# Kernel tuning notes

Measured on AMD Instinct MI355X. Metric: run time of the kernel, lower is better.

Reference implementation:

```python
import jax, jax.numpy as jnp
import numpy as np

NUM_EXPERTS = 8
EMBED_DIM = 1024
BATCH, SEQ = 4, 2048


def setup_inputs() -> dict:
    key = jax.random.key(0)
    k1, k2, k3 = jax.random.split(key, 3)
    E_symb = jax.random.normal(k1, (BATCH, SEQ, EMBED_DIM), dtype=jnp.float32)
    gate_w = jax.random.normal(k2, (EMBED_DIM, NUM_EXPERTS), dtype=jnp.float32) * 0.02
    gate_b = jnp.zeros((NUM_EXPERTS,), dtype=jnp.float32)
    expert_w = jax.random.normal(k3, (NUM_EXPERTS, EMBED_DIM, EMBED_DIM), dtype=jnp.float32) * 0.02
    return {"E_symb": E_symb, "gate_w": gate_w, "gate_b": gate_b,
            "expert_w": expert_w, "k": 2}


def reference(E_symb, gate_w, gate_b, expert_w, k):
    B, S, D = E_symb.shape
    E = expert_w.shape[0]
    x = E_symb.reshape(-1, D)                       # [T, D]
    logits = x @ gate_w + gate_b                    # [T, E]
    probs = jax.nn.softmax(logits.astype(jnp.float32), axis=-1)
    # top-k selection; NOTE: original renormalizes routing_weights but never
    # applies them to expert outputs -> combine is an UNWEIGHTED sum.
    _, sel = jax.lax.top_k(probs, k)                # [T, k]
    mask = jax.nn.one_hot(sel, E, dtype=x.dtype).sum(axis=1)  # [T, E] in {0,1}
    # dense grouped-GEMM then masked combine (replaces per-expert gather/scatter loop)
    y = jnp.einsum('td,edf->tef', x, expert_w)      # [T, E, D]
    out = jnp.einsum('tef,te->tf', y, mask)         # [T, D]
    return out.reshape(B, S, D)
```

## Files before the change

### kernel.cpp

```cpp
#include <hip/hip_runtime.h>
#include <hip/hip_bf16.h>
#include <stdint.h>

#define T_TOK 8192
#define DIM   1024
#define NEXP  8
#define BM    128
#define BN    128
#define BK2   32

typedef __bf16 bf16_t;
typedef bf16_t bf16x8 __attribute__((ext_vector_type(8)));
typedef bf16_t bf16x4 __attribute__((ext_vector_type(4)));
typedef float  f32x4  __attribute__((ext_vector_type(4)));

#define WS_CNT    0
#define CIDX(p)   ((p) << 4)
#define WS_LIST   8192
#define WS_XBF    (4u << 20)
#define WS_W2     (20u << 20)
#define WS_NEED_PSUM ((size_t)76 << 20)

__device__ const int d_PA[28] = {0,0,0,0,0,0,0,1,1,1,1,1,1,2,2,2,2,2,3,3,3,3,4,4,4,5,5,6};
__device__ const int d_PB[28] = {1,2,3,4,5,6,7,2,3,4,5,6,7,3,4,5,6,7,4,5,6,7,5,6,7,6,7,7};

__device__ __forceinline__ void gload16(const void* g, void* l) {
    __builtin_amdgcn_global_load_lds(
        (const __attribute__((address_space(1))) unsigned int*)g,
        (__attribute__((address_space(3))) unsigned int*)l, 16, 0, 0);
}

__device__ __forceinline__ int swz32(int r, int k) {
    return ((r * BK2 + k) * 2) ^ (((r >> 1) & 3) << 4);
}

#define WAITCNT_VM0()   do { asm volatile("s_waitcnt vmcnt(0)" ::: "memory"); \
                             __builtin_amdgcn_sched_barrier(0); } while (0)
#define WAITCNT_VM4()   do { asm volatile("s_waitcnt vmcnt(4)" ::: "memory"); \
                             __builtin_amdgcn_sched_barrier(0); } while (0)
#define WAITCNT_LGKM0() do { asm volatile("s_waitcnt lgkmcnt(0)" ::: "memory"); \
                             __builtin_amdgcn_sched_barrier(0); } while (0)
#define BARRIER()       do { __builtin_amdgcn_s_barrier(); \
                             __builtin_amdgcn_sched_barrier(0); } while (0)

template <int PSUM>
__global__ __launch_bounds__(256) void fused_pre(const float* __restrict__ x,
                                                 const float* __restrict__ gw,
                                                 const float* __restrict__ gb,
                                                 const float* __restrict__ ew,
                                                 bf16_t* __restrict__ xbf,
                                                 bf16_t* __restrict__ w2,
                                                 int* __restrict__ cnt,
                                                 int* __restrict__ list) {
    __shared__ __align__(16) float sh[NEXP * DIM];
    int bx  = blockIdx.x;
    int tid = threadIdx.x;
    if (bx < 1024) {
        float4 gb0 = *(const float4*)gb;
        float4 gb1 = *(const float4*)(gb + 4);
        float gbl[8] = {gb0.x, gb0.y, gb0.z, gb0.w, gb1.x, gb1.y, gb1.z, gb1.w};
        float* gwt = sh;
        const float4* gw4 = (const float4*)gw;
        #pragma unroll
        for (int i = 0; i < 8; i++) {
            int f4 = tid + i * 256;
            float4 v = gw4[f4];
            int d  = f4 >> 1;
            int e0 = (f4 & 1) * 4;
            gwt[(e0 + 0) * DIM + d] = v.x;
            gwt[(e0 + 1) * DIM + d] = v.y;
            gwt[(e0 + 2) * DIM + d] = v.z;
            gwt[(e0 + 3) * DIM + d] = v.w;
        }
        __syncthreads();
        int wid  = tid >> 6;
        int lane = tid & 63;
        const float4* gwt4 = (const float4*)gwt;
        for (int tt = 0; tt < 2; tt++) {
            int t = bx * 8 + wid * 2 + tt;
            const float4* xr4 = (const float4*)(x + (size_t)t * DIM);
            float acc[NEXP] = {};
            #pragma unroll
            for (int j = 0; j < 4; j++) {
                int c4 = j * 64 + lane;
                float4 v = xr4[c4];
                bf16x4 b;
                b[0] = (bf16_t)v.x; b[1] = (bf16_t)v.y;
                b[2] = (bf16_t)v.z; b[3] = (bf16_t)v.w;
                *(bf16x4*)(xbf + (size_t)t * DIM + c4 * 4) = b;
                #pragma unroll
                for (int e = 0; e < NEXP; e++) {
                    float4 g = gwt4[e * 256 + c4];
                    acc[e] += v.x * g.x + v.y * g.y + v.z * g.z + v.w * g.w;
                }
            }
            for (int off = 32; off >= 1; off >>= 1)
                #pragma unroll
                for (int e = 0; e < NEXP; e++)
                    acc[e] += __shfl_xor(acc[e], off, 64);
            if (lane == 0) {
                float logit[NEXP];
                #pragma unroll
                for (int e = 0; e < NEXP; e++) logit[e] = acc[e] + gbl[e];
                int b1 = 0; float best = logit[0];
                for (int e = 1; e < NEXP; e++) if (logit[e] > best) { best = logit[e]; b1 = e; }
                int b2 = -1; float best2 = -3.0e38f;
                for (int e = 0; e < NEXP; e++) {
                    if (e == b1) continue;
                    if (logit[e] > best2) { best2 = logit[e]; b2 = e; }
                }
                int a = min(b1, b2), bb = max(b1, b2);
                int p = a * 8 + bb;
                int pos = atomicAdd(&cnt[CIDX(p)], 1);
                list[p * T_TOK + pos] = t;
            }
        }
    } else {
        int bz  = bx - 1024;
        int g   = bz >> 8;
        int rem = bz & 255;
        int f0  = (rem & 15) * 64;
        int d0  = (rem >> 4) * 64;
        float (*tile)[65] = (float (*)[65])sh;
        int a = PSUM ? d_PA[g] : g;
        int b = PSUM ? d_PB[g] : g;
        const float* s1 = ew + ((size_t)a * DIM + d0) * DIM + f0;
        const float* s2 = ew + ((size_t)b * DIM + d0) * DIM + f0;
        int fl = (tid & 15) * 4;
        int dl = tid >> 4;
        #pragma unroll
        for (int i = 0; i < 4; i++) {
            int d = dl + i * 16;
            float4 u = *(const float4*)(s1 + (size_t)d * DIM + fl);
            if (PSUM) {
                float4 v = *(const float4*)(s2 + (size_t)d * DIM + fl);
                u.x += v.x; u.y += v.y; u.z += v.z; u.w += v.w;
            }
            tile[d][fl + 0] = u.x; tile[d][fl + 1] = u.y;
            tile[d][fl + 2] = u.z; tile[d][fl + 3] = u.w;
        }
        __syncthreads();
        bf16_t* dst = w2 + ((size_t)g * DIM + f0) * DIM + d0;
        int dl2 = (tid & 7) * 8;
        int fl2 = tid >> 3;
        #pragma unroll
        for (int i = 0; i < 2; i++) {
            int f = fl2 + i * 32;
            bf16x8 o;
            #pragma unroll
            for (int c = 0; c < 8; c++) o[c] = (bf16_t)tile[dl2 + c][f];
            *(bf16x8*)(dst + (size_t)f * DIM + dl2) = o;
        }
    }
}

template <int PSUM>
__global__ __launch_bounds__(256, 4) void moe_gemm(const bf16_t* __restrict__ xbf,
                                                   const bf16_t* __restrict__ wsrc,
                                                   const int* __restrict__ cnt,
                                                   const int* __restrict__ list,
                                                   float* __restrict__ out) {
    __shared__ __align__(16) bf16_t As[2][BM * BK2];
    __shared__ __align__(16) bf16_t Bs[2][BN * BK2];
    __shared__ int toks[BM];
    __shared__ int s_desc[128];
    __shared__ int s_ntile;
    int tid  = threadIdx.x;
    int lane = tid & 63;
    int wv   = tid >> 6;
    int wm   = wv >> 1, wn = wv & 1;

    if (tid < 64) {
        int c  = cnt[CIDX(tid)];
        int tp = (c + BM - 1) >> 7;
        int pre = 0, tot = 0;
        for (int i = 0; i < 64; i++) {
            int v = __shfl(tp, i, 64);
            if (i < tid) pre += v;
            tot += v;
        }
        for (int j = 0; j < tp; j++)
            s_desc[pre + j] = tid | ((j * BM) << 8);
        if (tid == 0) s_ntile = tot;
    }
    __syncthreads();
    int nwork = s_ntile * (DIM / BN);
    int q = nwork >> 3, r = nwork & 7;
    int xcd  = blockIdx.x & 7;
    int slot = blockIdx.x >> 3;
    int share = q + (xcd < r ? 1 : 0);
    if (slot >= share) return;
    int w = xcd * q + min(xcd, r) + slot;

    int dsc = s_desc[w >> 3];
    int n0  = (w & 7) * BN;
    int p   = dsc & 63;
    int m0  = dsc >> 8;
    int e1  = p >> 3, e2 = p & 7;
    int cp  = cnt[CIDX(p)];
    int valid = min(BM, cp - m0);
    if (tid < BM) toks[tid] = list[p * T_TOK + m0 + min(tid, valid - 1)];
    __syncthreads();

    const bf16_t* asrc[2];
    #pragma unroll
    for (int i = 0; i < 2; i++) {
        int c = i * 256 + tid;
        int rr = c >> 2, js = (c & 3) ^ ((rr >> 1) & 3);
        asrc[i] = xbf + (size_t)toks[rr] * DIM + js * 8;
    }

    f32x4 acc[4][4] = {};
    int lr = lane & 15;
    int lk = (lane >> 4) * 8;

    if (PSUM) {
        const bf16_t* bsrc[2];
        int pk = e1 * 7 - (e1 * (e1 - 1)) / 2 + (e2 - e1 - 1);
        const bf16_t* bb = wsrc + (size_t)pk * DIM * DIM;
        #pragma unroll
        for (int i = 0; i < 2; i++) {
            int c = i * 256 + tid;
            int rr = c >> 2, js = (c & 3) ^ ((rr >> 1) & 3);
            bsrc[i] = bb + (size_t)(n0 + rr) * DIM + js * 8;
        }
        #pragma unroll
        for (int i = 0; i < 2; i++)
            gload16(asrc[i], &As[0][(i * 256 + wv * 64) * 8]);
        #pragma unroll
        for (int i = 0; i < 2; i++)
            gload16(bsrc[i], &Bs[0][(i * 256 + wv * 64) * 8]);

        for (int ks = 0; ks < DIM / BK2; ks++) {
            int cur = ks & 1;
            if (ks < DIM / BK2 - 1) {
                int k1 = (ks + 1) * BK2;
                #pragma unroll
                for (int i = 0; i < 2; i++)
                    gload16(asrc[i] + k1, &As[cur ^ 1][(i * 256 + wv * 64) * 8]);
                #pragma unroll
                for (int i = 0; i < 2; i++)
                    gload16(bsrc[i] + k1, &Bs[cur ^ 1][(i * 256 + wv * 64) * 8]);
                WAITCNT_VM4();
            } else {
                WAITCNT_VM0();
            }
            BARRIER();
            const char* Ab = (const char*)As[cur];
            const char* Bb = (const char*)Bs[cur];
            bf16x8 af[4], bfr[4];
            #pragma unroll
            for (int mf = 0; mf < 4; mf++)
                af[mf] = *(const bf16x8*)(Ab + swz32(wm * 64 + mf * 16 + lr, lk));
            #pragma unroll
            for (int nf = 0; nf < 4; nf++)
                bfr[nf] = *(const bf16x8*)(Bb + swz32(wn * 64 + nf * 16 + lr, lk));
            #pragma unroll
            for (int mf = 0; mf < 4; mf++)
                #pragma unroll
                for (int nf = 0; nf < 4; nf++)
                    acc[mf][nf] = __builtin_amdgcn_mfma_f32_16x16x32_bf16(
                        af[mf], bfr[nf], acc[mf][nf], 0, 0, 0);
            BARRIER();
        }
    } else {
        const bf16_t* wt1 = wsrc + (size_t)e1 * DIM * DIM;
        const bf16_t* wt2 = wsrc + (size_t)e2 * DIM * DIM;
        for (int ks = 0; ks < DIM / BK2; ks++) {
            int k0 = ks * BK2;
            #pragma unroll
            for (int i = 0; i < 2; i++)
                gload16(asrc[i] + k0, &As[0][(i * 256 + wv * 64) * 8]);
            #pragma unroll
            for (int i = 0; i < 2; i++) {
                int c = i * 256 + tid;
                int f = c >> 2, j = c & 3;
                const bf16_t* s1 = wt1 + (size_t)(n0 + f) * DIM + k0 + j * 8;
                const bf16_t* s2 = wt2 + (size_t)(n0 + f) * DIM + k0 + j * 8;
                bf16x8 u = *(const bf16x8*)s1, w2v = *(const bf16x8*)s2, o;
                #pragma unroll
                for (int t = 0; t < 8; t++) o[t] = (bf16_t)((float)u[t] + (float)w2v[t]);
                *(bf16x8*)((char*)Bs[0] + swz32(f, j * 8)) = o;
            }
            WAITCNT_LGKM0();
            WAITCNT_VM0();
            BARRIER();
            const char* Ab = (const char*)As[0];
            const char* Bb = (const char*)Bs[0];
            bf16x8 af[4], bfr[4];
            #pragma unroll
            for (int mf = 0; mf < 4; mf++)
                af[mf] = *(const bf16x8*)(Ab + swz32(wm * 64 + mf * 16 + lr, lk));
            #pragma unroll
            for (int nf = 0; nf < 4; nf++)
                bfr[nf] = *(const bf16x8*)(Bb + swz32(wn * 64 + nf * 16 + lr, lk));
            #pragma unroll
            for (int mf = 0; mf < 4; mf++)
                #pragma unroll
                for (int nf = 0; nf < 4; nf++)
                    acc[mf][nf] = __builtin_amdgcn_mfma_f32_16x16x32_bf16(
                        af[mf], bfr[nf], acc[mf][nf], 0, 0, 0);
            BARRIER();
        }
    }

    #pragma unroll
    for (int mf = 0; mf < 4; mf++) {
        #pragma unroll
        for (int reg = 0; reg < 4; reg++) {
            int rl = wm * 64 + mf * 16 + (lane >> 4) * 4 + reg;
            if (rl < valid) {
                size_t trow = (size_t)toks[rl] * DIM;
                #pragma unroll
                for (int nf = 0; nf < 4; nf++)
                    out[trow + n0 + wn * 64 + nf * 16 + lr] = acc[mf][nf][reg];
            }
        }
    }
}

extern "C" void kernel_launch(void* const* d_in, const int* in_sizes, int n_in,
                              void* d_out, int out_size, void* d_ws, size_t ws_size,
                              hipStream_t stream) {
    const float* x  = (const float*)d_in[0];
    const float* gw = (const float*)d_in[1];
    const float* gb = (const float*)d_in[2];
    const float* ew = (const float*)d_in[3];
    float* out = (float*)d_out;
    char* ws = (char*)d_ws;
    int*    cnt  = (int*)(ws + WS_CNT);
    int*    list = (int*)(ws + WS_LIST);
    bf16_t* xbf  = (bf16_t*)(ws + WS_XBF);
    bf16_t* w2   = (bf16_t*)(ws + WS_W2);
    bool psum = (ws_size >= WS_NEED_PSUM);

    hipMemsetAsync(d_ws, 0, 8192, stream);
    if (psum) {
        fused_pre<1><<<dim3(1024 + 28 * 256), 256, 0, stream>>>(x, gw, gb, ew,
                                                                xbf, w2, cnt, list);
        moe_gemm<1><<<dim3(1024), 256, 0, stream>>>(xbf, w2, cnt, list, out);
    } else {
        fused_pre<0><<<dim3(1024 + 8 * 256), 256, 0, stream>>>(x, gw, gb, ew,
                                                               xbf, w2, cnt, list);
        moe_gemm<0><<<dim3(1024), 256, 0, stream>>>(xbf, w2, cnt, list, out);
    }
}
```

Before: 72.70 us.

## Build pair-sum expert weights from one shared tile read of all experts

The pair-sum weight prep now has each block load a 32x64 slice from all 8 experts once, convert it to bf16 in LDS, and emit all 28 pairwise sums. Previously each of the 28 pairs re-read two fp32 expert tiles, so expert weight traffic was far higher. Routing blocks now handle 32 tokens each instead of 8, which cuts the number of gate-weight transposes into LDS. The memset is replaced by a tiny zeroing kernel. Pair sums are now formed from bf16-rounded operands rather than fp32, a small precision change.

```diff
diff --git a/kernel.cpp b/kernel.cpp
--- a/kernel.cpp
+++ b/kernel.cpp
@@ -8,10 +8,12 @@
 #define BM    128
 #define BN    128
 #define BK2   32
+#define NR_ROUTE 256
 
 typedef __bf16 bf16_t;
 typedef bf16_t bf16x8 __attribute__((ext_vector_type(8)));
 typedef bf16_t bf16x4 __attribute__((ext_vector_type(4)));
+typedef bf16_t bf16x2 __attribute__((ext_vector_type(2)));
 typedef float  f32x4  __attribute__((ext_vector_type(4)));
 
 #define WS_CNT    0
@@ -42,6 +44,10 @@
                              __builtin_amdgcn_sched_barrier(0); } while (0)
 #define BARRIER()       do { __builtin_amdgcn_s_barrier(); \
                              __builtin_amdgcn_sched_barrier(0); } while (0)
+
+__global__ void zero_cnt(int4* cnt4) {
+    cnt4[threadIdx.x] = int4{0, 0, 0, 0};
+}
 
 template <int PSUM>
 __global__ __launch_bounds__(256) void fused_pre(const float* __restrict__ x,
@@ -55,7 +61,7 @@
     __shared__ __align__(16) float sh[NEXP * DIM];
     int bx  = blockIdx.x;
     int tid = threadIdx.x;
-    if (bx < 1024) {
+    if (bx < NR_ROUTE) {
         float4 gb0 = *(const float4*)gb;
         float4 gb1 = *(const float4*)(gb + 4);
         float gbl[8] = {gb0.x, gb0.y, gb0.z, gb0.w, gb1.x, gb1.y, gb1.z, gb1.w};
@@ -76,8 +82,8 @@
         int wid  = tid >> 6;
         int lane = tid & 63;
         const float4* gwt4 = (const float4*)gwt;
-        for (int tt = 0; tt < 2; tt++) {
-            int t = bx * 8 + wid * 2 + tt;
+        for (int tt = 0; tt < 8; tt++) {
+            int t = bx * 32 + wid * 8 + tt;
             const float4* xr4 = (const float4*)(x + (size_t)t * DIM);
             float acc[NEXP] = {};
             #pragma unroll
@@ -115,27 +121,57 @@
                 list[p * T_TOK + pos] = t;
             }
         }
+    } else if (PSUM) {
+        int bz = bx - NR_ROUTE;
+        int f0 = (bz & 15) * 64;
+        int d0 = (bz >> 4) * 32;
+        typedef bf16_t (*TileT)[64][32];
+        TileT T = (TileT)sh;
+        int dp = (tid & 15) * 2;
+        int f4 = tid >> 4;
+        #pragma unroll
+        for (int e = 0; e < 8; e++) {
+            const float* b0 = ew + ((size_t)e * DIM + d0 + dp) * DIM + f0 + f4 * 4;
+            float4 u0 = *(const float4*)b0;
+            float4 u1 = *(const float4*)(b0 + DIM);
+            float a0[4] = {u0.x, u0.y, u0.z, u0.w};
+            float a1[4] = {u1.x, u1.y, u1.z, u1.w};
+            #pragma unroll
+            for (int j = 0; j < 4; j++) {
+                bf16x2 w;
+                w[0] = (bf16_t)a0[j];
+                w[1] = (bf16_t)a1[j];
+                *(bf16x2*)&T[e][f4 * 4 + j][dp] = w;
+            }
+        }
+        __syncthreads();
+        const int PA[28] = {0,0,0,0,0,0,0,1,1,1,1,1,1,2,2,2,2,2,3,3,3,3,4,4,4,5,5,6};
+        const int PB[28] = {1,2,3,4,5,6,7,2,3,4,5,6,7,3,4,5,6,7,4,5,6,7,5,6,7,6,7,7};
+        int f  = tid >> 2;
+        int dd = (tid & 3) * 8;
+        #pragma unroll
+        for (int pk = 0; pk < 28; pk++) {
+            bf16x8 u = *(const bf16x8*)&T[PA[pk]][f][dd];
+            bf16x8 v = *(const bf16x8*)&T[PB[pk]][f][dd];
+            bf16x8 o;
+            #pragma unroll
+            for (int i = 0; i < 8; i++) o[i] = (bf16_t)((float)u[i] + (float)v[i]);
+            *(bf16x8*)(w2 + (size_t)pk * DIM * DIM + (size_t)(f0 + f) * DIM + d0 + dd) = o;
+        }
     } else {
-        int bz  = bx - 1024;
+        int bz  = bx - NR_ROUTE;
         int g   = bz >> 8;
         int rem = bz & 255;
         int f0  = (rem & 15) * 64;
         int d0  = (rem >> 4) * 64;
         float (*tile)[65] = (float (*)[65])sh;
-        int a = PSUM ? d_PA[g] : g;
-        int b = PSUM ? d_PB[g] : g;
-        const float* s1 = ew + ((size_t)a * DIM + d0) * DIM + f0;
-        const float* s2 = ew + ((size_t)b * DIM + d0) * DIM + f0;
+        const float* s1 = ew + ((size_t)g * DIM + d0) * DIM + f0;
         int fl = (tid & 15) * 4;
         int dl = tid >> 4;
         #pragma unroll
         for (int i = 0; i < 4; i++) {
             int d = dl + i * 16;
             float4 u = *(const float4*)(s1 + (size_t)d * DIM + fl);
-            if (PSUM) {
-                float4 v = *(const float4*)(s2 + (size_t)d * DIM + fl);
-                u.x += v.x; u.y += v.y; u.z += v.z; u.w += v.w;
-            }
             tile[d][fl + 0] = u.x; tile[d][fl + 1] = u.y;
             tile[d][fl + 2] = u.z; tile[d][fl + 3] = u.w;
         }
@@ -334,14 +370,14 @@
     bf16_t* w2   = (bf16_t*)(ws + WS_W2);
     bool psum = (ws_size >= WS_NEED_PSUM);
 
-    hipMemsetAsync(d_ws, 0, 8192, stream);
+    zero_cnt<<<dim3(1), 256, 0, stream>>>((int4*)cnt);
     if (psum) {
-        fused_pre<1><<<dim3(1024 + 28 * 256), 256, 0, stream>>>(x, gw, gb, ew,
-                                                                xbf, w2, cnt, list);
+        fused_pre<1><<<dim3(NR_ROUTE + 512), 256, 0, stream>>>(x, gw, gb, ew,
+                                                               xbf, w2, cnt, list);
         moe_gemm<1><<<dim3(1024), 256, 0, stream>>>(xbf, w2, cnt, list, out);
     } else {
-        fused_pre<0><<<dim3(1024 + 8 * 256), 256, 0, stream>>>(x, gw, gb, ew,
-                                                               xbf, w2, cnt, list);
+        fused_pre<0><<<dim3(NR_ROUTE + 8 * 256), 256, 0, stream>>>(x, gw, gb, ew,
+                                                                   xbf, w2, cnt, list);
         moe_gemm<0><<<dim3(1024), 256, 0, stream>>>(xbf, w2, cnt, list, out);
     }
 }
```

After: 76.33 us. +5.0%, slower.

## Split pair-sum weight build into transpose pass plus bf16 pairsum kernel

Applied to the files above, without the earlier changes.

Instead of reading two fp32 expert weight matrices per pair (28 pairs) and transposing, the pre-kernel now transposes and converts each of the 8 experts once to bf16, writing into the output buffer as scratch. A separate pairsum kernel then adds bf16 pairs to build the 28 summed matrices. This cuts fp32 global reads from 56 matrices to 8, at the cost of an extra launch, bf16 rounding before the summation, and reusing d_out as temporary storage. The memset is also replaced by a tiny zeroing kernel.

```diff
diff --git a/kernel.cpp b/kernel.cpp
--- a/kernel.cpp
+++ b/kernel.cpp
@@ -43,15 +43,18 @@
 #define BARRIER()       do { __builtin_amdgcn_s_barrier(); \
                              __builtin_amdgcn_sched_barrier(0); } while (0)
 
-template <int PSUM>
-__global__ __launch_bounds__(256) void fused_pre(const float* __restrict__ x,
-                                                 const float* __restrict__ gw,
-                                                 const float* __restrict__ gb,
-                                                 const float* __restrict__ ew,
-                                                 bf16_t* __restrict__ xbf,
-                                                 bf16_t* __restrict__ w2,
-                                                 int* __restrict__ cnt,
-                                                 int* __restrict__ list) {
+__global__ void zero_cnt(int4* cnt4) {
+    cnt4[threadIdx.x] = int4{0, 0, 0, 0};
+}
+
+__global__ __launch_bounds__(256) void pre1(const float* __restrict__ x,
+                                            const float* __restrict__ gw,
+                                            const float* __restrict__ gb,
+                                            const float* __restrict__ ew,
+                                            bf16_t* __restrict__ xbf,
+                                            bf16_t* __restrict__ wt,
+                                            int* __restrict__ cnt,
+                                            int* __restrict__ list) {
     __shared__ __align__(16) float sh[NEXP * DIM];
     int bx  = blockIdx.x;
     int tid = threadIdx.x;
@@ -122,25 +125,18 @@
         int f0  = (rem & 15) * 64;
         int d0  = (rem >> 4) * 64;
         float (*tile)[65] = (float (*)[65])sh;
-        int a = PSUM ? d_PA[g] : g;
-        int b = PSUM ? d_PB[g] : g;
-        const float* s1 = ew + ((size_t)a * DIM + d0) * DIM + f0;
-        const float* s2 = ew + ((size_t)b * DIM + d0) * DIM + f0;
+        const float* s1 = ew + ((size_t)g * DIM + d0) * DIM + f0;
         int fl = (tid & 15) * 4;
         int dl = tid >> 4;
         #pragma unroll
         for (int i = 0; i < 4; i++) {
             int d = dl + i * 16;
             float4 u = *(const float4*)(s1 + (size_t)d * DIM + fl);
-            if (PSUM) {
-                float4 v = *(const float4*)(s2 + (size_t)d * DIM + fl);
-                u.x += v.x; u.y += v.y; u.z += v.z; u.w += v.w;
-            }
             tile[d][fl + 0] = u.x; tile[d][fl + 1] = u.y;
             tile[d][fl + 2] = u.z; tile[d][fl + 3] = u.w;
         }
         __syncthreads();
-        bf16_t* dst = w2 + ((size_t)g * DIM + f0) * DIM + d0;
+        bf16_t* dst = wt + ((size_t)g * DIM + f0) * DIM + d0;
         int dl2 = (tid & 7) * 8;
         int fl2 = tid >> 3;
         #pragma unroll
@@ -151,6 +147,26 @@
             for (int c = 0; c < 8; c++) o[c] = (bf16_t)tile[dl2 + c][f];
             *(bf16x8*)(dst + (size_t)f * DIM + dl2) = o;
         }
+    }
+}
+
+__global__ __launch_bounds__(256) void pairsum(const bf16_t* __restrict__ wt,
+                                               bf16_t* __restrict__ wsum) {
+    int bz = blockIdx.x;
+    int pk = bz >> 7;
+    int cx = bz & 127;
+    int tid = threadIdx.x;
+    const bf16x8* wa = (const bf16x8*)(wt + (size_t)d_PA[pk] * DIM * DIM);
+    const bf16x8* wb = (const bf16x8*)(wt + (size_t)d_PB[pk] * DIM * DIM);
+    bf16x8*       wo = (bf16x8*)(wsum + (size_t)pk * DIM * DIM);
+    int base = cx * 1024 + tid;
+    #pragma unroll
+    for (int it = 0; it < 4; it++) {
+        int c = base + it * 256;
+        bf16x8 u = wa[c], v = wb[c], o;
+        #pragma unroll
+        for (int i = 0; i < 8; i++) o[i] = (bf16_t)((float)u[i] + (float)v[i]);
+        wo[c] = o;
     }
 }
 
@@ -334,14 +350,14 @@
     bf16_t* w2   = (bf16_t*)(ws + WS_W2);
     bool psum = (ws_size >= WS_NEED_PSUM);
 
-    hipMemsetAsync(d_ws, 0, 8192, stream);
+    zero_cnt<<<dim3(1), 256, 0, stream>>>((int4*)cnt);
     if (psum) {
-        fused_pre<1><<<dim3(1024 + 28 * 256), 256, 0, stream>>>(x, gw, gb, ew,
-                                                                xbf, w2, cnt, list);
+        bf16_t* wt_tmp = (bf16_t*)d_out;
+        pre1<<<dim3(3072), 256, 0, stream>>>(x, gw, gb, ew, xbf, wt_tmp, cnt, list);
+        pairsum<<<dim3(3584), 256, 0, stream>>>(wt_tmp, w2);
         moe_gemm<1><<<dim3(1024), 256, 0, stream>>>(xbf, w2, cnt, list, out);
     } else {
-        fused_pre<0><<<dim3(1024 + 8 * 256), 256, 0, stream>>>(x, gw, gb, ew,
-                                                               xbf, w2, cnt, list);
+        pre1<<<dim3(3072), 256, 0, stream>>>(x, gw, gb, ew, xbf, w2, cnt, list);
         moe_gemm<0><<<dim3(1024), 256, 0, stream>>>(xbf, w2, cnt, list, out);
     }
 }
```

Measured after the change: 71.77 us. About the same (-1.3%).
